# Kernel optimization log

Hardware: AMD Instinct MI355X
Metric: run time of the kernel (lower is better)

Reference implementation:

```python
import jax, jax.numpy as jnp
import numpy as np

H = 1024   # hidden_size
NH = 16    # num_heads
HD = H // NH
B, S = 2, 2048


def setup_inputs() -> dict:
    key = jax.random.key(0)
    ks = jax.random.split(key, 6)
    std = 0.02
    x = jax.random.normal(ks[0], (B, S, H), dtype=jnp.float32)
    w_qkv = jax.random.normal(ks[1], (3 * H, H), dtype=jnp.float32) * std
    b_qkv = jnp.zeros((3 * H,), dtype=jnp.float32)
    ln_g = jnp.ones((H,), dtype=jnp.float32)
    ln_b = jnp.zeros((H,), dtype=jnp.float32)
    w_ent = jax.random.normal(ks[2], (1, H), dtype=jnp.float32) * std
    b_ent = jnp.zeros((1,), dtype=jnp.float32)
    w_out = jax.random.normal(ks[3], (H, H), dtype=jnp.float32) * std
    b_out = jnp.zeros((H,), dtype=jnp.float32)
    return {"x": x, "ln_g": ln_g, "ln_b": ln_b, "w_qkv": w_qkv, "b_qkv": b_qkv,
            "w_ent": w_ent, "b_ent": b_ent, "w_out": w_out, "b_out": b_out}


def reference(x, ln_g, ln_b, w_qkv, b_qkv, w_ent, b_ent, w_out, b_out):
    b, s, h = x.shape
    scale = 1.0 / jnp.sqrt(jnp.float32(HD))
    TEMP = 0.1  # fixed softmax temperature

    # LayerNorm (eps=1e-6)
    mu = jnp.mean(x, axis=-1, keepdims=True)
    var = jnp.mean(jnp.square(x - mu), axis=-1, keepdims=True)
    xn = (x - mu) / jnp.sqrt(var + 1e-6) * ln_g + ln_b

    # QKV projection -> [B, S, 3, NH, HD] -> q,k,v each [B, NH, S, HD]
    qkv = xn @ w_qkv.T + b_qkv
    qkv = qkv.reshape(b, s, 3, NH, HD).transpose(2, 0, 3, 1, 4)
    q, k, v = qkv[0], qkv[1], qkv[2]

    # Scaled causal scores [B, NH, S, S]
    scores = jnp.einsum('bhqd,bhkd->bhqk', q, k) * scale
    causal = jnp.tril(jnp.ones((s, s), dtype=bool))
    scores = jnp.where(causal[None, None], scores, -jnp.inf)

    # Sharpened softmax (temperature 0.1); dropout is identity in eval
    probs = jax.nn.softmax(scores / TEMP, axis=-1)

    # Entropy gate over keys: sigmoid proj on post-LN x, clamped [0.1, 2.0]
    gate = jax.nn.sigmoid(xn @ w_ent.T + b_ent)        # [B, S, 1]
    gate = jnp.clip(gate, 0.1, 2.0)[:, None, None, :, 0]  # [B, 1, 1, S]
    probs = probs * gate

    # Weighted values -> merge heads -> output projection, scaled by 0.1
    out = jnp.einsum('bhqk,bhkd->bhqd', probs, v)
    out = out.transpose(0, 2, 1, 3).reshape(b, s, h)
    return (out @ w_out.T + b_out) * 0.1
```

## Files before the change

### kernel.cpp

```cpp
#include <hip/hip_runtime.h>

typedef __bf16 bf16x8 __attribute__((ext_vector_type(8)));
typedef float floatx4 __attribute__((ext_vector_type(4)));
typedef unsigned short u16;

#define LOG2E 1.44269504088896340736f
#define BF16_ONE 0x3F80u

static __device__ __forceinline__ float bf2f(u16 u) {
  union { unsigned int i; float f; } c; c.i = ((unsigned int)u) << 16; return c.f;
}
static __device__ __forceinline__ u16 f2bf(float f) {
  union { float f; unsigned int i; } c; c.f = f;
  unsigned int x = c.i;
  unsigned int r = (x >> 16) & 1u;
  x += 0x7fffu + r;
  return (u16)(x >> 16);
}
static __device__ __forceinline__ u16 f2bf_rne(float f) {
  __bf16 h = (__bf16)f;
  union { __bf16 h; u16 u; } c; c.h = h; return c.u;
}
static __device__ __forceinline__ float fast_exp2(float x) {
#if __has_builtin(__builtin_amdgcn_exp2f)
  return __builtin_amdgcn_exp2f(x);
#else
  return exp2f(x);
#endif
}
static __device__ __forceinline__ float ldp(const void* p, int i, bool isbf) {
  return isbf ? bf2f(((const u16*)p)[i]) : ((const float*)p)[i];
}

__global__ __launch_bounds__(256) void conv2_kernel(
    const void* __restrict__ src0, u16* __restrict__ dst0, int n8_0,
    const void* __restrict__ src1, u16* __restrict__ dst1, int n8_1,
    const u16* __restrict__ probe)
{
  bool isbf = (probe[0] == BF16_ONE);
  int i = blockIdx.x * 256 + threadIdx.x;
  const void* src = src0; u16* dst = dst0;
  if (i >= n8_0) { i -= n8_0; src = src1; dst = dst1; if (i >= n8_1) return; }
  if (isbf) {
    ((uint4*)dst)[i] = ((const uint4*)src)[i];
  } else {
    const float4* s = (const float4*)src;
    float4 a = s[2 * i], b = s[2 * i + 1];
    u16 o[8] = {f2bf(a.x), f2bf(a.y), f2bf(a.z), f2bf(a.w),
                f2bf(b.x), f2bf(b.y), f2bf(b.z), f2bf(b.w)};
    *(uint4*)(&dst[8 * i]) = *(uint4*)o;
  }
}

static __device__ __forceinline__ float blockSum(float v, float* red, int wave, int lane) {
  #pragma unroll
  for (int o = 32; o > 0; o >>= 1) v += __shfl_xor(v, o);
  __syncthreads();
  if (lane == 0) red[wave] = v;
  __syncthreads();
  return red[0] + red[1] + red[2] + red[3];
}

__global__ __launch_bounds__(256) void ln_gate_kernel(
    const void* __restrict__ x, const void* __restrict__ g, const void* __restrict__ bta,
    const void* __restrict__ w_ent, const void* __restrict__ b_ent,
    u16* __restrict__ xn, float* __restrict__ gate, const u16* __restrict__ probe)
{
  __shared__ float red[4];
  bool isbf = (probe[0] == BF16_ONE);
  int row = blockIdx.x;
  int tid = threadIdx.x;
  int wave = tid >> 6, lane = tid & 63;

  float v[4];
  #pragma unroll
  for (int i = 0; i < 4; ++i) {
    size_t idx = (size_t)row * 1024 + tid + 256 * i;
    v[i] = isbf ? bf2f(((const u16*)x)[idx]) : ((const float*)x)[idx];
  }

  float mu = blockSum(v[0] + v[1] + v[2] + v[3], red, wave, lane) * (1.0f / 1024.0f);

  float vs = 0.f;
  #pragma unroll
  for (int i = 0; i < 4; ++i) { float d = v[i] - mu; vs += d * d; }
  float var = blockSum(vs, red, wave, lane) * (1.0f / 1024.0f);
  float rstd = rsqrtf(var + 1e-6f);

  float gp = 0.f;
  #pragma unroll
  for (int i = 0; i < 4; ++i) {
    int col = tid + 256 * i;
    float xv = (v[i] - mu) * rstd * ldp(g, col, isbf) + ldp(bta, col, isbf);
    xn[(size_t)row * 1024 + col] = f2bf(xv);
    gp += xv * ldp(w_ent, col, isbf);
  }
  float tot = blockSum(gp, red, wave, lane);
  if (tid == 0) {
    float z = tot + ldp(b_ent, 0, isbf);
    float sg = 1.0f / (1.0f + exp2f(-z * LOG2E));
    gate[row] = fminf(fmaxf(sg, 0.1f), 2.0f);
  }
}

#define GEMM_STAGE(Abase, Wbase) \
  { \
    int lrow = lane >> 3; \
    int scb = ((lane & 7) ^ lrow) * 8; \
    _Pragma("unroll") \
    for (int it = 0; it < 4; ++it) { \
      int chunk = wave * 4 + it; \
      int row = chunk * 8 + lrow; \
      __builtin_amdgcn_global_load_lds( \
        (const __attribute__((address_space(1))) void*)&Abase[(size_t)(m0 + row) * K + k0 + scb], \
        (__attribute__((address_space(3))) void*)&As[chunk * 512], 16, 0, 0); \
      __builtin_amdgcn_global_load_lds( \
        (const __attribute__((address_space(1))) void*)&Wbase[(size_t)(n0 + row) * K + k0 + scb], \
        (__attribute__((address_space(3))) void*)&Ws[chunk * 512], 16, 0, 0); \
    } \
  }

#define GEMM_COMPUTE() \
  _Pragma("unroll") \
  for (int kk = 0; kk < 64; kk += 32) { \
    int kkb = kk >> 3; \
    bf16x8 af[4], bfr[4]; \
    _Pragma("unroll") \
    for (int i = 0; i < 4; ++i) \
      af[i] = *(const bf16x8*)(&As[(wm + 16 * i + lr) * 64 + ((kkb + lg) ^ (lr & 7)) * 8]); \
    _Pragma("unroll") \
    for (int j = 0; j < 4; ++j) \
      bfr[j] = *(const bf16x8*)(&Ws[(wn + 16 * j + lr) * 64 + ((kkb + lg) ^ (lr & 7)) * 8]); \
    _Pragma("unroll") \
    for (int i = 0; i < 4; ++i) \
      _Pragma("unroll") \
      for (int j = 0; j < 4; ++j) \
        acc[i][j] = __builtin_amdgcn_mfma_f32_16x16x32_bf16(af[i], bfr[j], acc[i][j], 0, 0, 0); \
  }

__global__ __launch_bounds__(256) void gemm_bt_kernel(
    const u16* __restrict__ A, const u16* __restrict__ W, const void* __restrict__ bias,
    u16* __restrict__ C, int M, int N, int K, const u16* __restrict__ probe)
{
  __shared__ __align__(16) u16 As[128 * 64];
  __shared__ __align__(16) u16 Ws[128 * 64];
  int m0 = blockIdx.y * 128, n0 = blockIdx.x * 128;
  int tid = threadIdx.x, wave = tid >> 6, lane = tid & 63;
  int lr = lane & 15, lg = lane >> 4;
  int wm = (wave >> 1) * 64, wn = (wave & 1) * 64;

  floatx4 acc[4][4];
  #pragma unroll
  for (int i = 0; i < 4; ++i)
    #pragma unroll
    for (int j = 0; j < 4; ++j)
      #pragma unroll
      for (int r = 0; r < 4; ++r) acc[i][j][r] = 0.f;

  for (int k0 = 0; k0 < K; k0 += 64) {
    GEMM_STAGE(A, W)
    __syncthreads();
    GEMM_COMPUTE()
    __syncthreads();
  }

  bool isbf = (probe[0] == BF16_ONE);
  #pragma unroll
  for (int j = 0; j < 4; ++j) {
    int n = n0 + wn + 16 * j + lr;
    float bv = ldp(bias, n, isbf);
    #pragma unroll
    for (int i = 0; i < 4; ++i) {
      int mbase = m0 + wm + 16 * i + lg * 4;
      #pragma unroll
      for (int r = 0; r < 4; ++r)
        C[(size_t)(mbase + r) * N + n] = f2bf(acc[i][j][r] + bv);
    }
  }
}

__global__ __launch_bounds__(256) void gemm_out_kernel(
    const u16* __restrict__ A, const u16* __restrict__ W, const void* __restrict__ bias,
    void* __restrict__ C, int M, int N, int K, float scale, const u16* __restrict__ probe)
{
  __shared__ __align__(16) u16 As[128 * 64];
  __shared__ __align__(16) u16 Ws[128 * 64];
  int m0 = blockIdx.y * 128, n0 = blockIdx.x * 128;
  int tid = threadIdx.x, wave = tid >> 6, lane = tid & 63;
  int lr = lane & 15, lg = lane >> 4;
  int wm = (wave >> 1) * 64, wn = (wave & 1) * 64;

  floatx4 acc[4][4];
  #pragma unroll
  for (int i = 0; i < 4; ++i)
    #pragma unroll
    for (int j = 0; j < 4; ++j)
      #pragma unroll
      for (int r = 0; r < 4; ++r) acc[i][j][r] = 0.f;

  for (int k0 = 0; k0 < K; k0 += 64) {
    GEMM_STAGE(A, W)
    __syncthreads();
    GEMM_COMPUTE()
    __syncthreads();
  }

  bool isbf = (probe[0] == BF16_ONE);
  #pragma unroll
  for (int j = 0; j < 4; ++j) {
    int n = n0 + wn + 16 * j + lr;
    float bv = ldp(bias, n, isbf);
    #pragma unroll
    for (int i = 0; i < 4; ++i) {
      int mbase = m0 + wm + 16 * i + lg * 4;
      #pragma unroll
      for (int r = 0; r < 4; ++r) {
        float v = (acc[i][j][r] + bv) * scale;
        size_t idx = (size_t)(mbase + r) * N + n;
        if (isbf) ((u16*)C)[idx] = f2bf(v);
        else      ((float*)C)[idx] = v;
      }
    }
  }
}

#define PSTR 72
#define CEXP (1.25f * LOG2E)

template<bool DOA>
static __device__ __forceinline__ void tile_compute(
    const u16* __restrict__ Ks, const u16* __restrict__ Vt,
    u16* __restrict__ psB, u16* __restrict__ psA,
    const bf16x8* qfB, const bf16x8* qfA,
    floatx4* accOB, floatx4* accOA, float* lB, float* lA,
    const float* gv, bool diagB, bool diagA, int wave, int lr, int lg)
{
  #pragma unroll
  for (int jt = 0; jt < 4; ++jt) {
    floatx4 aB = {0.f, 0.f, 0.f, 0.f};
    floatx4 aA = {0.f, 0.f, 0.f, 0.f};
    __builtin_amdgcn_s_setprio(1);
    #pragma unroll
    for (int kk = 0; kk < 2; ++kk) {
      bf16x8 bk = *(const bf16x8*)(&Ks[(jt * 16 + lr) * 72 + kk * 32 + lg * 8]);
      aB = __builtin_amdgcn_mfma_f32_16x16x32_bf16(qfB[kk], bk, aB, 0, 0, 0);
      if (DOA) aA = __builtin_amdgcn_mfma_f32_16x16x32_bf16(qfA[kk], bk, aA, 0, 0, 0);
    }
    __builtin_amdgcn_s_setprio(0);
    int kg = jt * 16 + lr;
    #pragma unroll
    for (int r = 0; r < 4; ++r) {
      int qg = wave * 16 + lg * 4 + r;
      float eB = fast_exp2(aB[r] * CEXP);
      if (diagB && kg > qg) eB = 0.f;
      lB[r] += eB;
      psB[(lg * 4 + r) * PSTR + kg] = f2bf_rne(eB * gv[jt]);
      if (DOA) {
        float eA = fast_exp2(aA[r] * CEXP);
        if (diagA && kg > qg) eA = 0.f;
        lA[r] += eA;
        psA[(lg * 4 + r) * PSTR + kg] = f2bf_rne(eA * gv[jt]);
      }
    }
  }
  bf16x8 apB[2], apA[2];
  #pragma unroll
  for (int kk = 0; kk < 2; ++kk) {
    apB[kk] = *(const bf16x8*)(&psB[lr * PSTR + kk * 32 + lg * 8]);
    if (DOA) apA[kk] = *(const bf16x8*)(&psA[lr * PSTR + kk * 32 + lg * 8]);
  }
  __builtin_amdgcn_s_setprio(1);
  #pragma unroll
  for (int jt = 0; jt < 4; ++jt)
    #pragma unroll
    for (int kk = 0; kk < 2; ++kk) {
      bf16x8 bv = *(const bf16x8*)(&Vt[(jt * 16 + lr) * 72 + kk * 32 + lg * 8]);
      accOB[jt] = __builtin_amdgcn_mfma_f32_16x16x32_bf16(apB[kk], bv, accOB[jt], 0, 0, 0);
      if (DOA) accOA[jt] = __builtin_amdgcn_mfma_f32_16x16x32_bf16(apA[kk], bv, accOA[jt], 0, 0, 0);
    }
  __builtin_amdgcn_s_setprio(0);
}

__global__ __launch_bounds__(256) void attn_kernel(
    const u16* __restrict__ qkv, const float* __restrict__ gate, u16* __restrict__ out)
{
  __shared__ __align__(16) u16 Ks[64 * 72];
  __shared__ __align__(16) u16 Vt[64 * 72];
  __shared__ __align__(16) u16 Ps[2 * 4 * 16 * PSTR];

  int bid = blockIdx.x;
  int xcd = bid & 7, kb = bid >> 3;
  int bh = xcd * 4 + (kb >> 4);
  int pr = kb & 15;
  int h = bh & 15, b = bh >> 4;
  int tid = threadIdx.x, wave = tid >> 6, lane = tid & 63;
  int lr = lane & 15, lg = lane >> 4;
  const int RS = 3072;

  int tA = pr, tB = 31 - pr;

  bf16x8 qfA[2], qfB[2];
  int qrbA = b * 2048 + tA * 64 + wave * 16;
  int qrbB = b * 2048 + tB * 64 + wave * 16;
  #pragma unroll
  for (int kk = 0; kk < 2; ++kk) {
    qfA[kk] = *(const bf16x8*)(&qkv[(size_t)(qrbA + lr) * RS + h * 64 + kk * 32 + lg * 8]);
    qfB[kk] = *(const bf16x8*)(&qkv[(size_t)(qrbB + lr) * RS + h * 64 + kk * 32 + lg * 8]);
  }

  floatx4 accOA[4], accOB[4];
  float lA[4] = {0.f, 0.f, 0.f, 0.f}, lB[4] = {0.f, 0.f, 0.f, 0.f};
  #pragma unroll
  for (int jt = 0; jt < 4; ++jt)
    #pragma unroll
    for (int r = 0; r < 4; ++r) { accOA[jt][r] = 0.f; accOB[jt][r] = 0.f; }

  u16* psB = &Ps[(size_t)wave * 16 * PSTR];
  u16* psA = &Ps[(size_t)(4 + wave) * 16 * PSTR];

  int srow = tid >> 3, sc8 = (tid & 7) * 8;
  int vkey = tid & 63, vd0 = (tid >> 6) * 16;

  uint4 kp0, kp1, vp0, vp1;
  float gp[4], gv[4];

  {
    int krow0 = b * 2048;
    kp0 = *(const uint4*)(&qkv[(size_t)(krow0 + srow) * RS + 1024 + h * 64 + sc8]);
    kp1 = *(const uint4*)(&qkv[(size_t)(krow0 + 32 + srow) * RS + 1024 + h * 64 + sc8]);
    const u16* vrow = &qkv[(size_t)(krow0 + vkey) * RS + 2048 + h * 64 + vd0];
    vp0 = *(const uint4*)(vrow);
    vp1 = *(const uint4*)(vrow + 8);
    #pragma unroll
    for (int jt = 0; jt < 4; ++jt) gp[jt] = gate[krow0 + jt * 16 + lr];
  }

  for (int kt = 0; kt <= tB; ++kt) {
    __syncthreads();
    *(uint4*)(&Ks[srow * 72 + sc8]) = kp0;
    *(uint4*)(&Ks[(srow + 32) * 72 + sc8]) = kp1;
    {
      unsigned int ww[8] = {vp0.x, vp0.y, vp0.z, vp0.w, vp1.x, vp1.y, vp1.z, vp1.w};
      #pragma unroll
      for (int i = 0; i < 8; ++i) {
        Vt[(vd0 + 2 * i) * 72 + vkey]     = (u16)(ww[i] & 0xffffu);
        Vt[(vd0 + 2 * i + 1) * 72 + vkey] = (u16)(ww[i] >> 16);
      }
    }
    #pragma unroll
    for (int jt = 0; jt < 4; ++jt) gv[jt] = gp[jt];
    __syncthreads();

    if (kt < tB) {
      int krow0 = b * 2048 + (kt + 1) * 64;
      kp0 = *(const uint4*)(&qkv[(size_t)(krow0 + srow) * RS + 1024 + h * 64 + sc8]);
      kp1 = *(const uint4*)(&qkv[(size_t)(krow0 + 32 + srow) * RS + 1024 + h * 64 + sc8]);
      const u16* vrow = &qkv[(size_t)(krow0 + vkey) * RS + 2048 + h * 64 + vd0];
      vp0 = *(const uint4*)(vrow);
      vp1 = *(const uint4*)(vrow + 8);
      #pragma unroll
      for (int jt = 0; jt < 4; ++jt) gp[jt] = gate[krow0 + jt * 16 + lr];
    }

    bool diagB = (kt == tB), diagA = (kt == tA);
    if (kt <= tA)
      tile_compute<true>(Ks, Vt, psB, psA, qfB, qfA, accOB, accOA, lB, lA,
                         gv, diagB, diagA, wave, lr, lg);
    else
      tile_compute<false>(Ks, Vt, psB, psA, qfB, qfA, accOB, accOA, lB, lA,
                          gv, diagB, diagA, wave, lr, lg);
  }

  #pragma unroll
  for (int r = 0; r < 4; ++r) {
    float lvB = lB[r], lvA = lA[r];
    #pragma unroll
    for (int o = 1; o < 16; o <<= 1) { lvB += __shfl_xor(lvB, o); lvA += __shfl_xor(lvA, o); }
    lB[r] = 1.0f / fmaxf(lvB, 1e-30f);
    lA[r] = 1.0f / fmaxf(lvA, 1e-30f);
  }
  #pragma unroll
  for (int jt = 0; jt < 4; ++jt)
    #pragma unroll
    for (int r = 0; r < 4; ++r) {
      int mB = qrbB + lg * 4 + r;
      out[(size_t)mB * 1024 + h * 64 + jt * 16 + lr] = f2bf(accOB[jt][r] * lB[r]);
      int mA = qrbA + lg * 4 + r;
      out[(size_t)mA * 1024 + h * 64 + jt * 16 + lr] = f2bf(accOA[jt][r] * lA[r]);
    }
}

extern "C" void kernel_launch(void* const* d_in, const int* in_sizes, int n_in,
                              void* d_out, int out_size, void* d_ws, size_t ws_size,
                              hipStream_t stream) {
  const void* x     = d_in[0];
  const void* ln_g  = d_in[1];
  const void* ln_b  = d_in[2];
  const void* w_qkv = d_in[3];
  const void* b_qkv = d_in[4];
  const void* w_ent = d_in[5];
  const void* b_ent = d_in[6];
  const void* w_out = d_in[7];
  const void* b_out = d_in[8];
  const u16* probe = (const u16*)ln_g;

  char* ws = (char*)d_ws;
  float* gate    = (float*)(ws);
  u16* xc        = (u16*)(ws + (64u << 10));
  u16* qkvb      = (u16*)(ws + (64u << 10) + (8u << 20));
  u16* w_qkv_c   = (u16*)(ws + (64u << 10) + (32u << 20));
  u16* w_out_c   = (u16*)(ws + (64u << 10) + (38u << 20));

  conv2_kernel<<<2048, 256, 0, stream>>>(w_qkv, w_qkv_c, 393216,
                                         w_out, w_out_c, 131072, probe);

  ln_gate_kernel<<<4096, 256, 0, stream>>>(x, ln_g, ln_b, w_ent, b_ent, xc, gate, probe);
  gemm_bt_kernel<<<dim3(24, 32), 256, 0, stream>>>(xc, w_qkv_c, b_qkv, qkvb, 4096, 3072, 1024, probe);
  attn_kernel<<<512, 256, 0, stream>>>(qkvb, gate, xc );
  gemm_out_kernel<<<dim3(8, 32), 256, 0, stream>>>(xc, w_out_c, b_out, d_out, 4096, 1024, 1024, 0.1f, probe);
}
```

Baseline: 216.0 us.

## Fold entropy gate into V projection epilogue and transpose score MFMA layout

The per-key gate is now multiplied into the V columns in the QKV GEMM epilogue, so the attention kernel no longer loads gate values or multiplies probabilities by them. The score MFMA operands are swapped so each lane holds four consecutive keys for one query. This lets P be written to shared memory as packed 8-byte stores and reduces the row-sum to a single scalar per lane with fewer shuffles. Rounding V after gating shifts bf16 rounding slightly, and the GEMM epilogue gains extra gate loads for the V tiles.

```diff
diff --git a/kernel.cpp b/kernel.cpp
--- a/kernel.cpp
+++ b/kernel.cpp
@@ -140,7 +140,8 @@
 
 __global__ __launch_bounds__(256) void gemm_bt_kernel(
     const u16* __restrict__ A, const u16* __restrict__ W, const void* __restrict__ bias,
-    u16* __restrict__ C, int M, int N, int K, const u16* __restrict__ probe)
+    const float* __restrict__ gate, u16* __restrict__ C, int M, int N, int K,
+    const u16* __restrict__ probe)
 {
   __shared__ __align__(16) u16 As[128 * 64];
   __shared__ __align__(16) u16 Ws[128 * 64];
@@ -165,6 +166,14 @@
   }
 
   bool isbf = (probe[0] == BF16_ONE);
+  bool doGate = (n0 >= 2048);
+  float gm[4][4];
+  #pragma unroll
+  for (int i = 0; i < 4; ++i)
+    #pragma unroll
+    for (int r = 0; r < 4; ++r)
+      gm[i][r] = doGate ? gate[m0 + wm + 16 * i + lg * 4 + r] : 1.0f;
+
   #pragma unroll
   for (int j = 0; j < 4; ++j) {
     int n = n0 + wn + 16 * j + lr;
@@ -174,7 +183,7 @@
       int mbase = m0 + wm + 16 * i + lg * 4;
       #pragma unroll
       for (int r = 0; r < 4; ++r)
-        C[(size_t)(mbase + r) * N + n] = f2bf(acc[i][j][r] + bv);
+        C[(size_t)(mbase + r) * N + n] = f2bf((acc[i][j][r] + bv) * gm[i][r]);
     }
   }
 }
@@ -232,9 +241,10 @@
     const u16* __restrict__ Ks, const u16* __restrict__ Vt,
     u16* __restrict__ psB, u16* __restrict__ psA,
     const bf16x8* qfB, const bf16x8* qfA,
-    floatx4* accOB, floatx4* accOA, float* lB, float* lA,
-    const float* gv, bool diagB, bool diagA, int wave, int lr, int lg)
-{
+    floatx4* accOB, floatx4* accOA, float& lB, float& lA,
+    bool diagB, bool diagA, int wave, int lr, int lg)
+{
+  int qg = wave * 16 + lr;
   #pragma unroll
   for (int jt = 0; jt < 4; ++jt) {
     floatx4 aB = {0.f, 0.f, 0.f, 0.f};
@@ -243,25 +253,27 @@
     #pragma unroll
     for (int kk = 0; kk < 2; ++kk) {
       bf16x8 bk = *(const bf16x8*)(&Ks[(jt * 16 + lr) * 72 + kk * 32 + lg * 8]);
-      aB = __builtin_amdgcn_mfma_f32_16x16x32_bf16(qfB[kk], bk, aB, 0, 0, 0);
-      if (DOA) aA = __builtin_amdgcn_mfma_f32_16x16x32_bf16(qfA[kk], bk, aA, 0, 0, 0);
+      aB = __builtin_amdgcn_mfma_f32_16x16x32_bf16(bk, qfB[kk], aB, 0, 0, 0);
+      if (DOA) aA = __builtin_amdgcn_mfma_f32_16x16x32_bf16(bk, qfA[kk], aA, 0, 0, 0);
     }
     __builtin_amdgcn_s_setprio(0);
-    int kg = jt * 16 + lr;
+    int kbase = jt * 16 + lg * 4;
+    u16 pb[4], pa[4];
     #pragma unroll
     for (int r = 0; r < 4; ++r) {
-      int qg = wave * 16 + lg * 4 + r;
       float eB = fast_exp2(aB[r] * CEXP);
-      if (diagB && kg > qg) eB = 0.f;
-      lB[r] += eB;
-      psB[(lg * 4 + r) * PSTR + kg] = f2bf_rne(eB * gv[jt]);
+      if (diagB && (kbase + r) > qg) eB = 0.f;
+      lB += eB;
+      pb[r] = f2bf_rne(eB);
       if (DOA) {
         float eA = fast_exp2(aA[r] * CEXP);
-        if (diagA && kg > qg) eA = 0.f;
-        lA[r] += eA;
-        psA[(lg * 4 + r) * PSTR + kg] = f2bf_rne(eA * gv[jt]);
+        if (diagA && (kbase + r) > qg) eA = 0.f;
+        lA += eA;
+        pa[r] = f2bf_rne(eA);
       }
     }
+    *(uint2*)(&psB[lr * PSTR + kbase]) = *(uint2*)pb;
+    if (DOA) *(uint2*)(&psA[lr * PSTR + kbase]) = *(uint2*)pa;
   }
   bf16x8 apB[2], apA[2];
   #pragma unroll
@@ -282,7 +294,7 @@
 }
 
 __global__ __launch_bounds__(256) void attn_kernel(
-    const u16* __restrict__ qkv, const float* __restrict__ gate, u16* __restrict__ out)
+    const u16* __restrict__ qkv, u16* __restrict__ out)
 {
   __shared__ __align__(16) u16 Ks[64 * 72];
   __shared__ __align__(16) u16 Vt[64 * 72];
@@ -309,7 +321,7 @@
   }
 
   floatx4 accOA[4], accOB[4];
-  float lA[4] = {0.f, 0.f, 0.f, 0.f}, lB[4] = {0.f, 0.f, 0.f, 0.f};
+  float lA = 0.f, lB = 0.f;
   #pragma unroll
   for (int jt = 0; jt < 4; ++jt)
     #pragma unroll
@@ -322,7 +334,6 @@
   int vkey = tid & 63, vd0 = (tid >> 6) * 16;
 
   uint4 kp0, kp1, vp0, vp1;
-  float gp[4], gv[4];
 
   {
     int krow0 = b * 2048;
@@ -331,8 +342,6 @@
     const u16* vrow = &qkv[(size_t)(krow0 + vkey) * RS + 2048 + h * 64 + vd0];
     vp0 = *(const uint4*)(vrow);
     vp1 = *(const uint4*)(vrow + 8);
-    #pragma unroll
-    for (int jt = 0; jt < 4; ++jt) gp[jt] = gate[krow0 + jt * 16 + lr];
   }
 
   for (int kt = 0; kt <= tB; ++kt) {
@@ -347,8 +356,6 @@
         Vt[(vd0 + 2 * i + 1) * 72 + vkey] = (u16)(ww[i] >> 16);
       }
     }
-    #pragma unroll
-    for (int jt = 0; jt < 4; ++jt) gv[jt] = gp[jt];
     __syncthreads();
 
     if (kt < tB) {
@@ -358,35 +365,33 @@
       const u16* vrow = &qkv[(size_t)(krow0 + vkey) * RS + 2048 + h * 64 + vd0];
       vp0 = *(const uint4*)(vrow);
       vp1 = *(const uint4*)(vrow + 8);
-      #pragma unroll
-      for (int jt = 0; jt < 4; ++jt) gp[jt] = gate[krow0 + jt * 16 + lr];
     }
 
     bool diagB = (kt == tB), diagA = (kt == tA);
     if (kt <= tA)
       tile_compute<true>(Ks, Vt, psB, psA, qfB, qfA, accOB, accOA, lB, lA,
-                         gv, diagB, diagA, wave, lr, lg);
+                         diagB, diagA, wave, lr, lg);
     else
       tile_compute<false>(Ks, Vt, psB, psA, qfB, qfA, accOB, accOA, lB, lA,
-                          gv, diagB, diagA, wave, lr, lg);
-  }
-
+                          diagB, diagA, wave, lr, lg);
+  }
+
+  lB += __shfl_xor(lB, 16); lB += __shfl_xor(lB, 32);
+  lA += __shfl_xor(lA, 16); lA += __shfl_xor(lA, 32);
+  float liB[4], liA[4];
   #pragma unroll
   for (int r = 0; r < 4; ++r) {
-    float lvB = lB[r], lvA = lA[r];
-    #pragma unroll
-    for (int o = 1; o < 16; o <<= 1) { lvB += __shfl_xor(lvB, o); lvA += __shfl_xor(lvA, o); }
-    lB[r] = 1.0f / fmaxf(lvB, 1e-30f);
-    lA[r] = 1.0f / fmaxf(lvA, 1e-30f);
+    liB[r] = 1.0f / fmaxf(__shfl(lB, lg * 4 + r), 1e-30f);
+    liA[r] = 1.0f / fmaxf(__shfl(lA, lg * 4 + r), 1e-30f);
   }
   #pragma unroll
   for (int jt = 0; jt < 4; ++jt)
     #pragma unroll
     for (int r = 0; r < 4; ++r) {
       int mB = qrbB + lg * 4 + r;
-      out[(size_t)mB * 1024 + h * 64 + jt * 16 + lr] = f2bf(accOB[jt][r] * lB[r]);
+      out[(size_t)mB * 1024 + h * 64 + jt * 16 + lr] = f2bf(accOB[jt][r] * liB[r]);
       int mA = qrbA + lg * 4 + r;
-      out[(size_t)mA * 1024 + h * 64 + jt * 16 + lr] = f2bf(accOA[jt][r] * lA[r]);
+      out[(size_t)mA * 1024 + h * 64 + jt * 16 + lr] = f2bf(accOA[jt][r] * liA[r]);
     }
 }
 
@@ -415,7 +420,7 @@
                                          w_out, w_out_c, 131072, probe);
 
   ln_gate_kernel<<<4096, 256, 0, stream>>>(x, ln_g, ln_b, w_ent, b_ent, xc, gate, probe);
-  gemm_bt_kernel<<<dim3(24, 32), 256, 0, stream>>>(xc, w_qkv_c, b_qkv, qkvb, 4096, 3072, 1024, probe);
-  attn_kernel<<<512, 256, 0, stream>>>(qkvb, gate, xc );
+  gemm_bt_kernel<<<dim3(24, 32), 256, 0, stream>>>(xc, w_qkv_c, b_qkv, gate, qkvb, 4096, 3072, 1024, probe);
+  attn_kernel<<<512, 256, 0, stream>>>(qkvb, xc );
   gemm_out_kernel<<<dim3(8, 32), 256, 0, stream>>>(xc, w_out_c, b_out, d_out, 4096, 1024, 1024, 0.1f, probe);
 }
```

Result: no change. 212.5 us (-1.6%).
